# Optimization experiments

Hardware: AMD Instinct MI355X
Metric: run time of the kernel (lower is better)

The kernel has to match this reference:

```python
import jax, jax.numpy as jnp
import numpy as np
import math

EPS = 1e-5

def _ln(x, g, b):
    m = jnp.mean(x, axis=-1, keepdims=True)
    v = jnp.mean((x - m) ** 2, axis=-1, keepdims=True)
    return (x - m) * jax.lax.rsqrt(v + EPS) * g + b

def _heads(t, H):
    B, T, C = t.shape
    return t.reshape(B, T, H, C // H).transpose(0, 2, 1, 3)  # [B,H,T,D]

def _merge(t):
    B, H, T, D = t.shape
    return t.transpose(0, 2, 1, 3).reshape(B, T, H * D)

def _self_attn(x, w, b, pw, pb, H):
    B, T, C = x.shape
    q, k, v = jnp.split(x @ w + b, 3, axis=-1)
    q, k, v = _heads(q, H), _heads(k, H), _heads(v, H)
    D = C // H
    att = jnp.einsum('bhqd,bhkd->bhqk', q, k) * (1.0 / math.sqrt(D))
    causal = jnp.tril(jnp.ones((T, T), bool))
    att = jnp.where(causal[None, None], att, jnp.float32(-jnp.inf))
    att = jax.nn.softmax(att, axis=-1)
    out = _merge(jnp.einsum('bhqk,bhkd->bhqd', att, v))
    return out @ pw + pb

def _cross_attn(enc, dec, w, b, pw, pb, H):
    B, Td, C = dec.shape
    q_dec = jnp.split(dec @ w + b, 3, axis=-1)[0]
    _, k_enc, v_enc = jnp.split(enc @ w + b, 3, axis=-1)
    q = _heads(q_dec, H); k = _heads(k_enc, H); v = _heads(v_enc, H)
    D = C // H
    att = jnp.einsum('bhqd,bhkd->bhqk', q, k) * (1.0 / math.sqrt(D))
    att = jax.nn.softmax(att, axis=-1)
    out = _merge(jnp.einsum('bhqk,bhkd->bhqd', att, v))
    return out @ pw + pb

def _block(x, encoder_embd,
           ln1_g, ln1_b, ln2_g, ln2_b, ln3_g, ln3_b,
           attn_w, attn_b, aproj_w, aproj_b,
           ca_w, ca_b, caproj_w, caproj_b,
           fc_w, fc_b, mproj_w, mproj_b,
           down_w, down_b, up_w, up_b, H=16):
    x = x + _self_attn(_ln(x, ln1_g, ln1_b), attn_w, attn_b, aproj_w, aproj_b, H)
    x = x + _cross_attn(encoder_embd, _ln(x, ln2_g, ln2_b), ca_w, ca_b, caproj_w, caproj_b, H)
    h = jax.nn.gelu(_ln(x, ln3_g, ln3_b) @ fc_w + fc_b, approximate=True) @ mproj_w + mproj_b
    adapt = jax.nn.gelu(h @ down_w + down_b, approximate=True) @ up_w + up_b + h  # Adapter residual
    return x + adapt


def setup_inputs() -> dict:
    key = jax.random.key(0)
    ks = jax.random.split(key, 12)
    B, T, Te, C, H = 4, 1024, 257, 1024, 16
    s = 0.02
    f32 = jnp.float32
    return {
        'x': jax.random.normal(ks[0], (B, T, C), f32),
        'encoder_embd': jax.random.normal(ks[1], (B, Te, C), f32),
        'prefix_embd': jnp.zeros((B, 1, C), f32),
        'ln1_g': jnp.ones((C,), f32), 'ln1_b': jnp.zeros((C,), f32),
        'ln2_g': jnp.ones((C,), f32), 'ln2_b': jnp.zeros((C,), f32),
        'ln3_g': jnp.ones((C,), f32), 'ln3_b': jnp.zeros((C,), f32),
        'attn_w': jax.random.normal(ks[2], (C, 3 * C), f32) * s,
        'attn_b': jnp.zeros((3 * C,), f32),
        'aproj_w': jax.random.normal(ks[3], (C, C), f32) * s,
        'aproj_b': jnp.zeros((C,), f32),
        'ca_w': jax.random.normal(ks[4], (C, 3 * C), f32) * s,
        'ca_b': jnp.zeros((3 * C,), f32),
        'caproj_w': jax.random.normal(ks[5], (C, C), f32) * s,
        'caproj_b': jnp.zeros((C,), f32),
        'fc_w': jax.random.normal(ks[6], (C, 4 * C), f32) * s,
        'fc_b': jnp.zeros((4 * C,), f32),
        'mproj_w': jax.random.normal(ks[7], (4 * C, C), f32) * s,
        'mproj_b': jnp.zeros((C,), f32),
        'down_w': jax.random.normal(ks[8], (C, C // 4), f32) * s,
        'down_b': jnp.zeros((C // 4,), f32),
        'up_w': jax.random.normal(ks[9], (C // 4, C), f32) * s,
        'up_b': jnp.zeros((C,), f32),
    }


def reference(x, encoder_embd, prefix_embd,
              ln1_g, ln1_b, ln2_g, ln2_b, ln3_g, ln3_b,
              attn_w, attn_b, aproj_w, aproj_b,
              ca_w, ca_b, caproj_w, caproj_b,
              fc_w, fc_b, mproj_w, mproj_b,
              down_w, down_b, up_w, up_b):
    # prefix_embd unused (peft='adapter')
    return _block(x, encoder_embd,
                  ln1_g, ln1_b, ln2_g, ln2_b, ln3_g, ln3_b,
                  attn_w, attn_b, aproj_w, aproj_b,
                  ca_w, ca_b, caproj_w, caproj_b,
                  fc_w, fc_b, mproj_w, mproj_b,
                  down_w, down_b, up_w, up_b)
```

## Files before the change

kernel.cpp:

```cpp
#include <hip/hip_runtime.h>

typedef __attribute__((ext_vector_type(8))) short short8v;
typedef __attribute__((ext_vector_type(8))) unsigned short ushort8v;
typedef __attribute__((ext_vector_type(4))) unsigned short ushort4v;
typedef __attribute__((ext_vector_type(4))) float f32x4;

__device__ __forceinline__ unsigned short f2b(float f) {
  unsigned int u = __float_as_uint(f);
  unsigned int r = (u + 0x7FFFu + ((u >> 16) & 1u)) >> 16;
  return (unsigned short)r;
}
__device__ __forceinline__ float b2f(unsigned short h) {
  return __uint_as_float(((unsigned int)h) << 16);
}
__device__ __forceinline__ float gelu_f(float x) {
  float z = 0.7978845608028654f * (x + 0.044715f * x * x * x);
  float e = __expf(2.0f * z);
  float t = 1.0f - 2.0f / (e + 1.0f);
  return 0.5f * x * (1.0f + t);
}
__device__ __forceinline__ int xcd_swz(int wgid, int nwg) {
  int q = nwg >> 3, r = nwg & 7;
  int xcd = wgid & 7, idx = wgid >> 3;
  return (xcd < r ? xcd * (q + 1) : r * (q + 1) + (xcd - r) * q) + idx;
}

__global__ __launch_bounds__(256) void k_wprep(
    const float* aw, unsigned short* awt,
    const float* apw, unsigned short* apwt,
    const float* cw, unsigned short* cwt,
    const float* cpw, unsigned short* cpwt,
    const float* fw, unsigned short* fwt,
    const float* mw, unsigned short* mwt,
    const float* dw, unsigned short* dwt,
    const float* uw, unsigned short* uwt,
    const float* enc, unsigned short* encb) {
  __shared__ float tile[64][65];
  int bid = blockIdx.x, t = threadIdx.x;
  const float* w; unsigned short* wt; int K, N, gx, l;
  if      (bid < 768)  { w = aw;  wt = awt;  K = 1024; N = 3072; gx = 48; l = bid; }
  else if (bid < 1024) { w = apw; wt = apwt; K = 1024; N = 1024; gx = 16; l = bid - 768; }
  else if (bid < 1792) { w = cw;  wt = cwt;  K = 1024; N = 3072; gx = 48; l = bid - 1024; }
  else if (bid < 2048) { w = cpw; wt = cpwt; K = 1024; N = 1024; gx = 16; l = bid - 1792; }
  else if (bid < 3072) { w = fw;  wt = fwt;  K = 1024; N = 4096; gx = 64; l = bid - 2048; }
  else if (bid < 4096) { w = mw;  wt = mwt;  K = 4096; N = 1024; gx = 16; l = bid - 3072; }
  else if (bid < 4160) { w = dw;  wt = dwt;  K = 1024; N = 256;  gx = 4;  l = bid - 4096; }
  else if (bid < 4224) { w = uw;  wt = uwt;  K = 256;  N = 1024; gx = 16; l = bid - 4160; }
  else {
    size_t i = ((size_t)(bid - 4224) * 256 + t) * 4;
    f32x4 v = *(const f32x4*)&enc[i];
    ushort4v o;
#pragma unroll
    for (int j = 0; j < 4; ++j) o[j] = f2b(v[j]);
    *(ushort4v*)&encb[i] = o;
    return;
  }
  int bx = l % gx, by = l / gx;
  int tn = bx * 64, tk = by * 64;
  int c = t & 63, r0 = t >> 6;
#pragma unroll
  for (int p = 0; p < 16; ++p) {
    int r = r0 + p * 4;
    tile[r][c] = w[(size_t)(tk + r) * N + tn + c];
  }
  __syncthreads();
#pragma unroll
  for (int p = 0; p < 16; ++p) {
    int r = r0 + p * 4;
    wt[(size_t)(tn + r) * K + tk + c] = f2b(tile[c][r]);
  }
}

__global__ __launch_bounds__(256) void k_ln(const float* __restrict__ in,
                                            const float* __restrict__ g,
                                            const float* __restrict__ b,
                                            unsigned short* __restrict__ out) {
  int row = blockIdx.x;
  const float* x = in + (size_t)row * 1024;
  int t = threadIdx.x;
  float v0 = x[t], v1 = x[t + 256], v2 = x[t + 512], v3 = x[t + 768];
  float s = v0 + v1 + v2 + v3;
  float s2 = v0 * v0 + v1 * v1 + v2 * v2 + v3 * v3;
#pragma unroll
  for (int m = 1; m < 64; m <<= 1) { s += __shfl_xor(s, m); s2 += __shfl_xor(s2, m); }
  __shared__ float rs[4], rs2[4];
  int w = t >> 6;
  if ((t & 63) == 0) { rs[w] = s; rs2[w] = s2; }
  __syncthreads();
  s = rs[0] + rs[1] + rs[2] + rs[3];
  s2 = rs2[0] + rs2[1] + rs2[2] + rs2[3];
  float mean = s * (1.0f / 1024.0f);
  float var = s2 * (1.0f / 1024.0f) - mean * mean;
  float rinv = rsqrtf(var + 1e-5f);
  unsigned short* o = out + (size_t)row * 1024;
  o[t]       = f2b((v0 - mean) * rinv * g[t]       + b[t]);
  o[t + 256] = f2b((v1 - mean) * rinv * g[t + 256] + b[t + 256]);
  o[t + 512] = f2b((v2 - mean) * rinv * g[t + 512] + b[t + 512]);
  o[t + 768] = f2b((v3 - mean) * rinv * g[t + 768] + b[t + 768]);
}

template <bool GELU, bool WF32, bool WBF16, int NRES, bool RES1B>
__global__ __launch_bounds__(256, 2) void k_g128r(
    const unsigned short* __restrict__ A, int lda,
    const unsigned short* __restrict__ W, int ldw,
    const float* __restrict__ bias,
    const float* __restrict__ res1, const unsigned short* __restrict__ res1b,
    const float* __restrict__ res2,
    float* __restrict__ outF, unsigned short* __restrict__ outB,
    int M, int N, int K, int nbx) {
  __shared__ unsigned short lds[32768];
  const int t = threadIdx.x;
  const int swz = xcd_swz(blockIdx.x, gridDim.x);
  const int tileM = (swz / nbx) * 128, tileN = (swz % nbx) * 128;
  const int lane = t & 63, w = t >> 6;
  const int wm = (w >> 1) * 64, wn = (w & 1) * 64;
  const int lr16 = lane & 15, kc4 = lane >> 4;

  const int sr = t >> 1, hb = t & 1;
  int gr = tileM + sr; if (gr >= M) gr = M - 1;
  const unsigned short* ga = A + (size_t)gr * lda + hb * 32;
  const unsigned short* gw = W + (size_t)(tileN + sr) * ldw + hb * 32;
  unsigned short* const wbA = &lds[sr * 64];
  const int wsl[4] = {((hb * 4 + 0) ^ (sr & 7)) * 8, ((hb * 4 + 1) ^ (sr & 7)) * 8,
                      ((hb * 4 + 2) ^ (sr & 7)) * 8, ((hb * 4 + 3) ^ (sr & 7)) * 8};

  f32x4 acc[4][4];
#pragma unroll
  for (int i = 0; i < 4; ++i)
#pragma unroll
    for (int j = 0; j < 4; ++j) acc[i][j] = f32x4{0.f, 0.f, 0.f, 0.f};

  const int nt = K >> 6;
  ushort8v raE[4], rbE[4], raO[4], rbO[4];

#define LOADT(T, ra, rb)                                      \
  do {                                                        \
    int ko = (T) << 6;                                        \
    _Pragma("unroll") for (int j = 0; j < 4; ++j) {           \
      ra[j] = *(const ushort8v*)(ga + ko + j * 8);            \
      rb[j] = *(const ushort8v*)(gw + ko + j * 8);            \
    }                                                         \
  } while (0)
#define WRITET(ra, rb, bsel)                                  \
  do {                                                        \
    unsigned short* dA = wbA + (bsel) * 16384;                \
    _Pragma("unroll") for (int j = 0; j < 4; ++j) {           \
      *(ushort8v*)(dA + wsl[j]) = ra[j];                      \
      *(ushort8v*)(dA + 8192 + wsl[j]) = rb[j];               \
    }                                                         \
  } while (0)
#define COMPUTE(bsel)                                                           \
  do {                                                                          \
    const int base = (bsel) * 16384;                                            \
    _Pragma("unroll") for (int ks = 0; ks < 2; ++ks) {                          \
      short8v bfr[4];                                                           \
      _Pragma("unroll") for (int n = 0; n < 4; ++n) {                           \
        int r = wn + n * 16 + lr16;                                             \
        int sl = ((ks * 4 + kc4) ^ (r & 7)) * 8;                                \
        bfr[n] = *(const short8v*)&lds[base + 8192 + r * 64 + sl];              \
      }                                                                         \
      _Pragma("unroll") for (int mi = 0; mi < 4; ++mi) {                        \
        int r = wm + mi * 16 + lr16;                                            \
        int sl = ((ks * 4 + kc4) ^ (r & 7)) * 8;                                \
        short8v af = *(const short8v*)&lds[base + r * 64 + sl];                 \
        _Pragma("unroll") for (int n = 0; n < 4; ++n)                           \
          acc[mi][n] =                                                          \
              __builtin_amdgcn_mfma_f32_16x16x32_bf16(af, bfr[n], acc[mi][n], 0, 0, 0); \
      }                                                                         \
    }                                                                           \
  } while (0)

  LOADT(0, raE, rbE);
  WRITET(raE, rbE, 0);
  if (nt > 1) LOADT(1, raO, rbO);
  __syncthreads();

  for (int T = 0; T < nt; T += 2) {
    if (T + 2 < nt) LOADT(T + 2, raE, rbE);
    COMPUTE(0);
    if (T + 1 < nt) WRITET(raO, rbO, 1);
    __syncthreads();
    if (T + 1 < nt) {
      if (T + 3 < nt) LOADT(T + 3, raO, rbO);
      COMPUTE(1);
      if (T + 2 < nt) WRITET(raE, rbE, 0);
      __syncthreads();
    }
  }
#undef LOADT
#undef WRITET
#undef COMPUTE

#pragma unroll
  for (int mi = 0; mi < 4; ++mi) {
#pragma unroll
    for (int n = 0; n < 4; ++n) {
      int col = tileN + wn + n * 16 + lr16;
      float bv = bias[col];
#pragma unroll
      for (int qi = 0; qi < 4; ++qi) {
        int row = tileM + wm + mi * 16 + kc4 * 4 + qi;
        if (row < M) {
          float v = acc[mi][n][qi] + bv;
          if (GELU) v = gelu_f(v);
          size_t o = (size_t)row * N + col;
          if (NRES >= 1) v += RES1B ? b2f(res1b[o]) : res1[o];
          if (NRES >= 2) v += res2[o];
          if (WF32) outF[o] = v;
          if (WBF16) outB[o] = f2b(v);
        }
      }
    }
  }
}

__global__ __launch_bounds__(256) void k_vtrans(const unsigned short* __restrict__ src,
                                                int src_stride, int src_off, int TB,
                                                unsigned short* __restrict__ dst, int dst_tstride) {
  __shared__ unsigned short tile[64][72];
  int tb = blockIdx.x, bh = blockIdx.y;
  int b = bh >> 4, h = bh & 15;
  int t = threadIdx.x;
  int r = t >> 2, c0 = (t & 3) * 16;
  int tok = tb * 64 + r; if (tok >= TB) tok = TB - 1;
  const unsigned short* s = src + (size_t)(b * TB + tok) * src_stride + src_off + h * 64 + c0;
  *(ushort8v*)&tile[r][c0] = *(const ushort8v*)s;
  *(ushort8v*)&tile[r][c0 + 8] = *(const ushort8v*)(s + 8);
  __syncthreads();
  unsigned short tmp[16];
#pragma unroll
  for (int j = 0; j < 16; ++j) tmp[j] = tile[c0 + j][r];
  unsigned short* dp = dst + ((size_t)bh * 64 + r) * dst_tstride + tb * 64 + c0;
  *(ushort8v*)dp = *(const ushort8v*)&tmp[0];
  *(ushort8v*)(dp + 8) = *(const ushort8v*)&tmp[8];
}

template <bool CAUSAL>
__global__ __launch_bounds__(256) void k_attn(
    const unsigned short* __restrict__ Qb, int q_stride,
    const unsigned short* __restrict__ Kb, int k_stride, int k_off, int TKR,
    const unsigned short* __restrict__ Vt, int vt_tstride,
    unsigned short* __restrict__ out, int Tk) {
  __shared__ unsigned short Kl[64 * 72];
  __shared__ unsigned short Vl[64 * 72];
  __shared__ unsigned short Pl[4][16 * 72];
  const int swz = xcd_swz(blockIdx.x, gridDim.x);
  int qb = swz & 15, bh = swz >> 4;
  int b = bh >> 4, h = bh & 15;
  int t = threadIdx.x, lane = t & 63, w = t >> 6;
  int g = lane >> 4, lc = lane & 15;

  int qrow_g = qb * 64 + w * 16 + lc;
  const unsigned short* qp = Qb + (size_t)(b * 1024 + qrow_g) * q_stride + h * 64 + g * 8;
  short8v aq0 = *(const short8v*)qp;
  short8v aq1 = *(const short8v*)(qp + 32);

  f32x4 o[4];
  float m_[4], l_[4];
#pragma unroll
  for (int dt = 0; dt < 4; ++dt) o[dt] = f32x4{0.f, 0.f, 0.f, 0.f};
#pragma unroll
  for (int r = 0; r < 4; ++r) { m_[r] = -3.0e38f; l_[r] = 0.0f; }

  int srow = t >> 2;
  int sc = (t & 3) * 16;
  int ntiles = CAUSAL ? (qb + 1) : ((Tk + 63) >> 6);

  for (int kt = 0; kt < ntiles; ++kt) {
    __syncthreads();
    {
      int kg = kt * 64 + srow;
      if (!CAUSAL && kg >= Tk) kg = Tk - 1;
      const unsigned short* ks = Kb + (size_t)(b * TKR + kg) * k_stride + k_off + h * 64 + sc;
      *(ushort8v*)&Kl[srow * 72 + sc]     = *(const ushort8v*)ks;
      *(ushort8v*)&Kl[srow * 72 + sc + 8] = *(const ushort8v*)(ks + 8);
      const unsigned short* vs = Vt + ((size_t)bh * 64 + srow) * vt_tstride + kt * 64 + sc;
      *(ushort8v*)&Vl[srow * 72 + sc]     = *(const ushort8v*)vs;
      *(ushort8v*)&Vl[srow * 72 + sc + 8] = *(const ushort8v*)(vs + 8);
    }
    __syncthreads();

    f32x4 s[4];
#pragma unroll
    for (int jt = 0; jt < 4; ++jt) {
      short8v bk0 = *(const short8v*)&Kl[(jt * 16 + lc) * 72 + g * 8];
      short8v bk1 = *(const short8v*)&Kl[(jt * 16 + lc) * 72 + g * 8 + 32];
      f32x4 acc = f32x4{0.f, 0.f, 0.f, 0.f};
      acc = __builtin_amdgcn_mfma_f32_16x16x32_bf16(aq0, bk0, acc, 0, 0, 0);
      acc = __builtin_amdgcn_mfma_f32_16x16x32_bf16(aq1, bk1, acc, 0, 0, 0);
      s[jt] = acc;
    }
#pragma unroll
    for (int jt = 0; jt < 4; ++jt)
#pragma unroll
      for (int r = 0; r < 4; ++r) {
        float sv = s[jt][r] * 0.125f;
        bool masked = CAUSAL ? (kt == qb && (jt * 16 + lc) > (w * 16 + g * 4 + r))
                             : (kt * 64 + jt * 16 + lc >= Tk);
        s[jt][r] = masked ? -3.0e38f : sv;
      }
    float f[4];
#pragma unroll
    for (int r = 0; r < 4; ++r) {
      float mx = fmaxf(fmaxf(s[0][r], s[1][r]), fmaxf(s[2][r], s[3][r]));
      mx = fmaxf(mx, __shfl_xor(mx, 1));
      mx = fmaxf(mx, __shfl_xor(mx, 2));
      mx = fmaxf(mx, __shfl_xor(mx, 4));
      mx = fmaxf(mx, __shfl_xor(mx, 8));
      float mnew = fmaxf(m_[r], mx);
      f[r] = __expf(m_[r] - mnew);
      m_[r] = mnew;
      float rsum = 0.0f;
#pragma unroll
      for (int jt = 0; jt < 4; ++jt) {
        float p = __expf(s[jt][r] - mnew);
        s[jt][r] = p;
        rsum += p;
      }
      rsum += __shfl_xor(rsum, 1);
      rsum += __shfl_xor(rsum, 2);
      rsum += __shfl_xor(rsum, 4);
      rsum += __shfl_xor(rsum, 8);
      l_[r] = l_[r] * f[r] + rsum;
    }
#pragma unroll
    for (int dt = 0; dt < 4; ++dt)
#pragma unroll
      for (int r = 0; r < 4; ++r) o[dt][r] *= f[r];
#pragma unroll
    for (int jt = 0; jt < 4; ++jt)
#pragma unroll
      for (int r = 0; r < 4; ++r)
        Pl[w][(g * 4 + r) * 72 + jt * 16 + lc] = f2b(s[jt][r]);
    short8v ap0 = *(const short8v*)&Pl[w][lc * 72 + g * 8];
    short8v ap1 = *(const short8v*)&Pl[w][lc * 72 + g * 8 + 32];
#pragma unroll
    for (int dt = 0; dt < 4; ++dt) {
      short8v bv0 = *(const short8v*)&Vl[(dt * 16 + lc) * 72 + g * 8];
      short8v bv1 = *(const short8v*)&Vl[(dt * 16 + lc) * 72 + g * 8 + 32];
      o[dt] = __builtin_amdgcn_mfma_f32_16x16x32_bf16(ap0, bv0, o[dt], 0, 0, 0);
      o[dt] = __builtin_amdgcn_mfma_f32_16x16x32_bf16(ap1, bv1, o[dt], 0, 0, 0);
    }
  }
  size_t orow = (size_t)(b * 1024 + qb * 64 + w * 16) * 1024 + h * 64;
#pragma unroll
  for (int r = 0; r < 4; ++r) {
    float inv = 1.0f / l_[r];
#pragma unroll
    for (int dt = 0; dt < 4; ++dt)
      out[orow + (size_t)(g * 4 + r) * 1024 + dt * 16 + lc] = f2b(o[dt][r] * inv);
  }
}

extern "C" void kernel_launch(void* const* d_in, const int* in_sizes, int n_in,
                              void* d_out, int out_size, void* d_ws, size_t ws_size,
                              hipStream_t stream) {
  (void)in_sizes; (void)n_in; (void)out_size; (void)ws_size;
  const float* x       = (const float*)d_in[0];
  const float* enc     = (const float*)d_in[1];
  const float* ln1_g   = (const float*)d_in[3];
  const float* ln1_b   = (const float*)d_in[4];
  const float* ln2_g   = (const float*)d_in[5];
  const float* ln2_b   = (const float*)d_in[6];
  const float* ln3_g   = (const float*)d_in[7];
  const float* ln3_b   = (const float*)d_in[8];
  const float* attn_w  = (const float*)d_in[9];
  const float* attn_b  = (const float*)d_in[10];
  const float* aproj_w = (const float*)d_in[11];
  const float* aproj_b = (const float*)d_in[12];
  const float* ca_w    = (const float*)d_in[13];
  const float* ca_b    = (const float*)d_in[14];
  const float* caproj_w= (const float*)d_in[15];
  const float* caproj_b= (const float*)d_in[16];
  const float* fc_w    = (const float*)d_in[17];
  const float* fc_b    = (const float*)d_in[18];
  const float* mproj_w = (const float*)d_in[19];
  const float* mproj_b = (const float*)d_in[20];
  const float* down_w  = (const float*)d_in[21];
  const float* down_b  = (const float*)d_in[22];
  const float* up_w    = (const float*)d_in[23];
  const float* up_b    = (const float*)d_in[24];
  float* out = (float*)d_out;
  char* ws = (char*)d_ws;

  const size_t O_WATTN = 0, O_WAPROJ = 6291456, O_WCA = 8388608, O_WCAPROJ = 14680064,
               O_WFC = 16777216, O_WMPROJ = 25165824, O_WDOWN = 33554432, O_WUP = 34078720,
               O_ENC = 34603008, O_LN = 36708352, O_BIG = 45096960,
               O_XRES = 78651392, O_ATTN = 112205824;

  unsigned short* wt_attn   = (unsigned short*)(ws + O_WATTN);
  unsigned short* wt_aproj  = (unsigned short*)(ws + O_WAPROJ);
  unsigned short* wt_ca     = (unsigned short*)(ws + O_WCA);
  unsigned short* wt_caproj = (unsigned short*)(ws + O_WCAPROJ);
  unsigned short* wt_fc     = (unsigned short*)(ws + O_WFC);
  unsigned short* wt_mproj  = (unsigned short*)(ws + O_WMPROJ);
  unsigned short* wt_down   = (unsigned short*)(ws + O_WDOWN);
  unsigned short* wt_up     = (unsigned short*)(ws + O_WUP);
  unsigned short* encbf     = (unsigned short*)(ws + O_ENC);
  unsigned short* lnout     = (unsigned short*)(ws + O_LN);
  unsigned short* hbf       = (unsigned short*)(ws + O_LN);
  unsigned short* qkvb      = (unsigned short*)(ws + O_BIG);
  unsigned short* vt_self   = (unsigned short*)(ws + O_BIG + 25165824);
  unsigned short* q2b       = (unsigned short*)(ws + O_BIG);
  unsigned short* kvb       = (unsigned short*)(ws + O_BIG + 8388608);
  unsigned short* vt_cross  = (unsigned short*)(ws + O_BIG + 12599296);
  unsigned short* caout     = (unsigned short*)(ws + O_BIG + 15220736);
  unsigned short* fcout     = (unsigned short*)(ws + O_BIG);
  float*          xres      = (float*)(ws + O_XRES);
  unsigned short* attnout   = (unsigned short*)(ws + O_ATTN);
  unsigned short* dmid      = (unsigned short*)(ws + O_ATTN);

  dim3 blk(256);

  k_wprep<<<dim3(5252), blk, 0, stream>>>(
      attn_w, wt_attn, aproj_w, wt_aproj, ca_w, wt_ca, caproj_w, wt_caproj,
      fc_w, wt_fc, mproj_w, wt_mproj, down_w, wt_down, up_w, wt_up, enc, encbf);

  k_ln<<<dim3(4096), blk, 0, stream>>>(x, ln1_g, ln1_b, lnout);
  k_g128r<false, false, true, 0, false><<<dim3(768), blk, 0, stream>>>(
      lnout, 1024, wt_attn, 1024, attn_b, nullptr, nullptr, nullptr, nullptr, qkvb,
      4096, 3072, 1024, 24);
  k_vtrans<<<dim3(16, 64), blk, 0, stream>>>(qkvb, 3072, 2048, 1024, vt_self, 1024);
  k_attn<true><<<dim3(1024), blk, 0, stream>>>(
      qkvb, 3072, qkvb, 3072, 1024, 1024, vt_self, 1024, attnout, 1024);
  k_g128r<false, true, false, 1, false><<<dim3(256), blk, 0, stream>>>(
      attnout, 1024, wt_aproj, 1024, aproj_b, x, nullptr, nullptr, xres, nullptr,
      4096, 1024, 1024, 8);

  k_ln<<<dim3(4096), blk, 0, stream>>>(xres, ln2_g, ln2_b, lnout);
  k_g128r<false, false, true, 0, false><<<dim3(256), blk, 0, stream>>>(
      lnout, 1024, wt_ca, 1024, ca_b, nullptr, nullptr, nullptr, nullptr, q2b,
      4096, 1024, 1024, 8);
  k_g128r<false, false, true, 0, false><<<dim3(144), blk, 0, stream>>>(
      encbf, 1024, wt_ca + (size_t)1024 * 1024, 1024, ca_b + 1024, nullptr, nullptr,
      nullptr, nullptr, kvb, 1028, 2048, 1024, 16);
  k_vtrans<<<dim3(5, 64), blk, 0, stream>>>(kvb, 2048, 1024, 257, vt_cross, 320);
  k_attn<false><<<dim3(1024), blk, 0, stream>>>(
      q2b, 1024, kvb, 2048, 0, 257, vt_cross, 320, caout, 257);
  k_g128r<false, true, false, 1, false><<<dim3(256), blk, 0, stream>>>(
      caout, 1024, wt_caproj, 1024, caproj_b, xres, nullptr, nullptr, xres, nullptr,
      4096, 1024, 1024, 8);

  k_ln<<<dim3(4096), blk, 0, stream>>>(xres, ln3_g, ln3_b, lnout);
  k_g128r<true, false, true, 0, false><<<dim3(1024), blk, 0, stream>>>(
      lnout, 1024, wt_fc, 1024, fc_b, nullptr, nullptr, nullptr, nullptr, fcout,
      4096, 4096, 1024, 32);
  k_g128r<false, false, true, 0, false><<<dim3(256), blk, 0, stream>>>(
      fcout, 4096, wt_mproj, 4096, mproj_b, nullptr, nullptr, nullptr, nullptr, hbf,
      4096, 1024, 4096, 8);

  k_g128r<true, false, true, 0, false><<<dim3(64), blk, 0, stream>>>(
      hbf, 1024, wt_down, 1024, down_b, nullptr, nullptr, nullptr, nullptr, dmid,
      4096, 256, 1024, 2);
  k_g128r<false, true, false, 2, true><<<dim3(256), blk, 0, stream>>>(
      dmid, 256, wt_up, 256, up_b, nullptr, hbf, xres, out, nullptr,
      4096, 1024, 256, 8);
}
```

Before: 456.2 us.

## Single-buffer GEMM LDS for higher occupancy and remap tiles per XCD

The 128x128 GEMM kernel moves from a double-buffered LDS tile (64KB) to a single buffer (32KB) and raises launch_bounds occupancy from 2 to 4 blocks per CU. The aim is to hide memory latency with more resident waves instead of intra-block double buffering. The cost is extra __syncthreads per K step, since writes and computes on the one buffer must now be serialised. A new tile mapping gives each XCD a contiguous 2D region of output tiles for better L2 reuse, falling back to the old swizzle when the grid shape does not divide evenly.

```diff
diff --git a/kernel.cpp b/kernel.cpp
--- a/kernel.cpp
+++ b/kernel.cpp
@@ -23,6 +23,20 @@
   int q = nwg >> 3, r = nwg & 7;
   int xcd = wgid & 7, idx = wgid >> 3;
   return (xcd < r ? xcd * (q + 1) : r * (q + 1) + (xcd - r) * q) + idx;
+}
+__device__ __forceinline__ void map_tile(int wgid, int nwg, int nbx, int& tm, int& tn) {
+  int nby = nwg / nbx;
+  if ((nwg & 7) == 0 && (nby & 3) == 0 && (nbx & 1) == 0) {
+    int x = wgid & 7, idx = wgid >> 3;
+    int rh = nby >> 2, rw = nbx >> 1;
+    int xr = x >> 1, xc = x & 1;
+    tm = xr * rh + idx / rw;
+    tn = xc * rw + idx % rw;
+  } else {
+    int swz = xcd_swz(wgid, nwg);
+    tm = swz / nbx;
+    tn = swz % nbx;
+  }
 }
 
 __global__ __launch_bounds__(256) void k_wprep(
@@ -100,7 +114,7 @@
 }
 
 template <bool GELU, bool WF32, bool WBF16, int NRES, bool RES1B>
-__global__ __launch_bounds__(256, 2) void k_g128r(
+__global__ __launch_bounds__(256, 4) void k_g128r(
     const unsigned short* __restrict__ A, int lda,
     const unsigned short* __restrict__ W, int ldw,
     const float* __restrict__ bias,
@@ -108,10 +122,11 @@
     const float* __restrict__ res2,
     float* __restrict__ outF, unsigned short* __restrict__ outB,
     int M, int N, int K, int nbx) {
-  __shared__ unsigned short lds[32768];
+  __shared__ unsigned short lds[16384];
   const int t = threadIdx.x;
-  const int swz = xcd_swz(blockIdx.x, gridDim.x);
-  const int tileM = (swz / nbx) * 128, tileN = (swz % nbx) * 128;
+  int tm, tn;
+  map_tile(blockIdx.x, gridDim.x, nbx, tm, tn);
+  const int tileM = tm * 128, tileN = tn * 128;
   const int lane = t & 63, w = t >> 6;
   const int wm = (w >> 1) * 64, wn = (w & 1) * 64;
   const int lr16 = lane & 15, kc4 = lane >> 4;
@@ -141,28 +156,26 @@
       rb[j] = *(const ushort8v*)(gw + ko + j * 8);            \
     }                                                         \
   } while (0)
-#define WRITET(ra, rb, bsel)                                  \
+#define WRITET(ra, rb)                                        \
   do {                                                        \
-    unsigned short* dA = wbA + (bsel) * 16384;                \
     _Pragma("unroll") for (int j = 0; j < 4; ++j) {           \
-      *(ushort8v*)(dA + wsl[j]) = ra[j];                      \
-      *(ushort8v*)(dA + 8192 + wsl[j]) = rb[j];               \
+      *(ushort8v*)(wbA + wsl[j]) = ra[j];                     \
+      *(ushort8v*)(wbA + 8192 + wsl[j]) = rb[j];              \
     }                                                         \
   } while (0)
-#define COMPUTE(bsel)                                                           \
+#define COMPUTE()                                                               \
   do {                                                                          \
-    const int base = (bsel) * 16384;                                            \
     _Pragma("unroll") for (int ks = 0; ks < 2; ++ks) {                          \
       short8v bfr[4];                                                           \
       _Pragma("unroll") for (int n = 0; n < 4; ++n) {                           \
         int r = wn + n * 16 + lr16;                                             \
         int sl = ((ks * 4 + kc4) ^ (r & 7)) * 8;                                \
-        bfr[n] = *(const short8v*)&lds[base + 8192 + r * 64 + sl];              \
+        bfr[n] = *(const short8v*)&lds[8192 + r * 64 + sl];                     \
       }                                                                         \
       _Pragma("unroll") for (int mi = 0; mi < 4; ++mi) {                        \
         int r = wm + mi * 16 + lr16;                                            \
         int sl = ((ks * 4 + kc4) ^ (r & 7)) * 8;                                \
-        short8v af = *(const short8v*)&lds[base + r * 64 + sl];                 \
+        short8v af = *(const short8v*)&lds[r * 64 + sl];                        \
         _Pragma("unroll") for (int n = 0; n < 4; ++n)                           \
           acc[mi][n] =                                                          \
               __builtin_amdgcn_mfma_f32_16x16x32_bf16(af, bfr[n], acc[mi][n], 0, 0, 0); \
@@ -171,19 +184,21 @@
   } while (0)
 
   LOADT(0, raE, rbE);
-  WRITET(raE, rbE, 0);
+  WRITET(raE, rbE);
   if (nt > 1) LOADT(1, raO, rbO);
   __syncthreads();
 
   for (int T = 0; T < nt; T += 2) {
     if (T + 2 < nt) LOADT(T + 2, raE, rbE);
-    COMPUTE(0);
-    if (T + 1 < nt) WRITET(raO, rbO, 1);
+    COMPUTE();
     __syncthreads();
     if (T + 1 < nt) {
+      WRITET(raO, rbO);
       if (T + 3 < nt) LOADT(T + 3, raO, rbO);
-      COMPUTE(1);
-      if (T + 2 < nt) WRITET(raE, rbE, 0);
+      __syncthreads();
+      COMPUTE();
+      __syncthreads();
+      if (T + 2 < nt) WRITET(raE, rbE);
       __syncthreads();
     }
   }
```

Result: slower. 793.9 us (+74.0%).

## Split-K the mproj and adapter-down GEMMs with a reduction kernel, add 2D XCD tile mapping

Applied to the files above, without the earlier changes.

The mproj GEMM (K=4096, 256 tiles) and the adapter down-projection (64 tiles) each split K four ways, write fp32 partials to a new workspace region, and a new reduction kernel sums them, adds bias, applies GELU where needed and writes bf16. This raises workgroup count so these small-tile-count GEMMs can fill the GPU, at the cost of extra fp32 partial traffic and an additional launch. A new tile mapper also assigns each XCD a contiguous 2D block of output tiles when the grid shape allows, aiming for better L2 reuse of A and W. The split path only runs if the workspace is large enough, otherwise the old path is used.

```diff
diff --git a/kernel.cpp b/kernel.cpp
--- a/kernel.cpp
+++ b/kernel.cpp
@@ -23,6 +23,20 @@
   int q = nwg >> 3, r = nwg & 7;
   int xcd = wgid & 7, idx = wgid >> 3;
   return (xcd < r ? xcd * (q + 1) : r * (q + 1) + (xcd - r) * q) + idx;
+}
+__device__ __forceinline__ void map_tile(int wgid, int nwg, int nbx, int& tm, int& tn) {
+  int nby = nwg / nbx;
+  if ((nwg & 7) == 0 && (nby & 3) == 0 && (nbx & 1) == 0) {
+    int x = wgid & 7, idx = wgid >> 3;
+    int rh = nby >> 2, rw = nbx >> 1;
+    int xr = x >> 1, xc = x & 1;
+    tm = xr * rh + idx / rw;
+    tn = xc * rw + idx % rw;
+  } else {
+    int swz = xcd_swz(wgid, nwg);
+    tm = swz / nbx;
+    tn = swz % nbx;
+  }
 }
 
 __global__ __launch_bounds__(256) void k_wprep(
@@ -99,7 +113,7 @@
   o[t + 768] = f2b((v3 - mean) * rinv * g[t + 768] + b[t + 768]);
 }
 
-template <bool GELU, bool WF32, bool WBF16, int NRES, bool RES1B>
+template <bool GELU, bool BIAS, bool WF32, bool WBF16, int NRES, bool RES1B>
 __global__ __launch_bounds__(256, 2) void k_g128r(
     const unsigned short* __restrict__ A, int lda,
     const unsigned short* __restrict__ W, int ldw,
@@ -107,19 +121,24 @@
     const float* __restrict__ res1, const unsigned short* __restrict__ res1b,
     const float* __restrict__ res2,
     float* __restrict__ outF, unsigned short* __restrict__ outB,
-    int M, int N, int K, int nbx) {
+    int M, int N, int K, int nbx, int splitk, size_t zO) {
   __shared__ unsigned short lds[32768];
   const int t = threadIdx.x;
-  const int swz = xcd_swz(blockIdx.x, gridDim.x);
-  const int tileM = (swz / nbx) * 128, tileN = (swz % nbx) * 128;
+  const int nsub = gridDim.x / splitk;
+  const int split = blockIdx.x / nsub;
+  const int sub = blockIdx.x % nsub;
+  int tm, tn;
+  map_tile(sub, nsub, nbx, tm, tn);
+  const int tileM = tm * 128, tileN = tn * 128;
+  const int Keff = K / splitk;
   const int lane = t & 63, w = t >> 6;
   const int wm = (w >> 1) * 64, wn = (w & 1) * 64;
   const int lr16 = lane & 15, kc4 = lane >> 4;
 
   const int sr = t >> 1, hb = t & 1;
   int gr = tileM + sr; if (gr >= M) gr = M - 1;
-  const unsigned short* ga = A + (size_t)gr * lda + hb * 32;
-  const unsigned short* gw = W + (size_t)(tileN + sr) * ldw + hb * 32;
+  const unsigned short* ga = A + (size_t)gr * lda + (size_t)split * Keff + hb * 32;
+  const unsigned short* gw = W + (size_t)(tileN + sr) * ldw + (size_t)split * Keff + hb * 32;
   unsigned short* const wbA = &lds[sr * 64];
   const int wsl[4] = {((hb * 4 + 0) ^ (sr & 7)) * 8, ((hb * 4 + 1) ^ (sr & 7)) * 8,
                       ((hb * 4 + 2) ^ (sr & 7)) * 8, ((hb * 4 + 3) ^ (sr & 7)) * 8};
@@ -130,7 +149,7 @@
 #pragma unroll
     for (int j = 0; j < 4; ++j) acc[i][j] = f32x4{0.f, 0.f, 0.f, 0.f};
 
-  const int nt = K >> 6;
+  const int nt = Keff >> 6;
   ushort8v raE[4], rbE[4], raO[4], rbO[4];
 
 #define LOADT(T, ra, rb)                                      \
@@ -191,12 +210,13 @@
 #undef WRITET
 #undef COMPUTE
 
+  if (WF32 && splitk > 1) outF += (size_t)split * zO;
 #pragma unroll
   for (int mi = 0; mi < 4; ++mi) {
 #pragma unroll
     for (int n = 0; n < 4; ++n) {
       int col = tileN + wn + n * 16 + lr16;
-      float bv = bias[col];
+      float bv = BIAS ? bias[col] : 0.0f;
 #pragma unroll
       for (int qi = 0; qi < 4; ++qi) {
         int row = tileM + wm + mi * 16 + kc4 * 4 + qi;
@@ -212,6 +232,22 @@
       }
     }
   }
+}
+
+template <bool GELU, int NM1>
+__global__ __launch_bounds__(256) void k_red(const float* __restrict__ p,
+                                             const float* __restrict__ bias,
+                                             unsigned short* __restrict__ ob, size_t S) {
+  size_t i = ((size_t)blockIdx.x * 256 + threadIdx.x) * 4;
+  f32x4 v = *(const f32x4*)&p[i];
+  v += *(const f32x4*)&p[i + S];
+  v += *(const f32x4*)&p[i + 2 * S];
+  v += *(const f32x4*)&p[i + 3 * S];
+  v += *(const f32x4*)&bias[i & NM1];
+  ushort4v o;
+#pragma unroll
+  for (int j = 0; j < 4; ++j) o[j] = f2b(GELU ? gelu_f(v[j]) : v[j]);
+  *(ushort4v*)&ob[i] = o;
 }
 
 __global__ __launch_bounds__(256) void k_vtrans(const unsigned short* __restrict__ src,
@@ -355,7 +391,7 @@
 extern "C" void kernel_launch(void* const* d_in, const int* in_sizes, int n_in,
                               void* d_out, int out_size, void* d_ws, size_t ws_size,
                               hipStream_t stream) {
-  (void)in_sizes; (void)n_in; (void)out_size; (void)ws_size;
+  (void)in_sizes; (void)n_in; (void)out_size;
   const float* x       = (const float*)d_in[0];
   const float* enc     = (const float*)d_in[1];
   const float* ln1_g   = (const float*)d_in[3];
@@ -386,7 +422,7 @@
   const size_t O_WATTN = 0, O_WAPROJ = 6291456, O_WCA = 8388608, O_WCAPROJ = 14680064,
                O_WFC = 16777216, O_WMPROJ = 25165824, O_WDOWN = 33554432, O_WUP = 34078720,
                O_ENC = 34603008, O_LN = 36708352, O_BIG = 45096960,
-               O_XRES = 78651392, O_ATTN = 112205824;
+               O_XRES = 78651392, O_ATTN = 112205824, O_PART = 121634816;
 
   unsigned short* wt_attn   = (unsigned short*)(ws + O_WATTN);
   unsigned short* wt_aproj  = (unsigned short*)(ws + O_WAPROJ);
@@ -409,6 +445,9 @@
   float*          xres      = (float*)(ws + O_XRES);
   unsigned short* attnout   = (unsigned short*)(ws + O_ATTN);
   unsigned short* dmid      = (unsigned short*)(ws + O_ATTN);
+  float*          part      = (float*)(ws + O_PART);
+
+  bool splitok = ws_size >= O_PART + 67108864;
 
   dim3 blk(256);
 
@@ -417,42 +456,58 @@
       fc_w, wt_fc, mproj_w, wt_mproj, down_w, wt_down, up_w, wt_up, enc, encbf);
 
   k_ln<<<dim3(4096), blk, 0, stream>>>(x, ln1_g, ln1_b, lnout);
-  k_g128r<false, false, true, 0, false><<<dim3(768), blk, 0, stream>>>(
+  k_g128r<false, true, false, true, 0, false><<<dim3(768), blk, 0, stream>>>(
       lnout, 1024, wt_attn, 1024, attn_b, nullptr, nullptr, nullptr, nullptr, qkvb,
-      4096, 3072, 1024, 24);
+      4096, 3072, 1024, 24, 1, 0);
   k_vtrans<<<dim3(16, 64), blk, 0, stream>>>(qkvb, 3072, 2048, 1024, vt_self, 1024);
   k_attn<true><<<dim3(1024), blk, 0, stream>>>(
       qkvb, 3072, qkvb, 3072, 1024, 1024, vt_self, 1024, attnout, 1024);
-  k_g128r<false, true, false, 1, false><<<dim3(256), blk, 0, stream>>>(
+  k_g128r<false, true, true, false, 1, false><<<dim3(256), blk, 0, stream>>>(
       attnout, 1024, wt_aproj, 1024, aproj_b, x, nullptr, nullptr, xres, nullptr,
-      4096, 1024, 1024, 8);
+      4096, 1024, 1024, 8, 1, 0);
 
   k_ln<<<dim3(4096), blk, 0, stream>>>(xres, ln2_g, ln2_b, lnout);
-  k_g128r<false, false, true, 0, false><<<dim3(256), blk, 0, stream>>>(
+  k_g128r<false, true, false, true, 0, false><<<dim3(256), blk, 0, stream>>>(
       lnout, 1024, wt_ca, 1024, ca_b, nullptr, nullptr, nullptr, nullptr, q2b,
-      4096, 1024, 1024, 8);
-  k_g128r<false, false, true, 0, false><<<dim3(144), blk, 0, stream>>>(
+      4096, 1024, 1024, 8, 1, 0);
+  k_g128r<false, true, false, true, 0, false><<<dim3(144), blk, 0, stream>>>(
       encbf, 1024, wt_ca + (size_t)1024 * 1024, 1024, ca_b + 1024, nullptr, nullptr,
-      nullptr, nullptr, kvb, 1028, 2048, 1024, 16);
+      nullptr, nullptr, kvb, 1028, 2048, 1024, 16, 1, 0);
   k_vtrans<<<dim3(5, 64), blk, 0, stream>>>(kvb, 2048, 1024, 257, vt_cross, 320);
   k_attn<false><<<dim3(1024), blk, 0, stream>>>(
       q2b, 1024, kvb, 2048, 0, 257, vt_cross, 320, caout, 257);
-  k_g128r<false, true, false, 1, false><<<dim3(256), blk, 0, stream>>>(
+  k_g128r<false, true, true, false, 1, false><<<dim3(256), blk, 0, stream>>>(
       caout, 1024, wt_caproj, 1024, caproj_b, xres, nullptr, nullptr, xres, nullptr,
-      4096, 1024, 1024, 8);
+      4096, 1024, 1024, 8, 1, 0);
 
   k_ln<<<dim3(4096), blk, 0, stream>>>(xres, ln3_g, ln3_b, lnout);
-  k_g128r<true, false, true, 0, false><<<dim3(1024), blk, 0, stream>>>(
+  k_g128r<true, true, false, true, 0, false><<<dim3(1024), blk, 0, stream>>>(
       lnout, 1024, wt_fc, 1024, fc_b, nullptr, nullptr, nullptr, nullptr, fcout,
-      4096, 4096, 1024, 32);
-  k_g128r<false, false, true, 0, false><<<dim3(256), blk, 0, stream>>>(
-      fcout, 4096, wt_mproj, 4096, mproj_b, nullptr, nullptr, nullptr, nullptr, hbf,
-      4096, 1024, 4096, 8);
-
-  k_g128r<true, false, true, 0, false><<<dim3(64), blk, 0, stream>>>(
-      hbf, 1024, wt_down, 1024, down_b, nullptr, nullptr, nullptr, nullptr, dmid,
-      4096, 256, 1024, 2);
-  k_g128r<false, true, false, 2, true><<<dim3(256), blk, 0, stream>>>(
+      4096, 4096, 1024, 32, 1, 0);
+  if (splitok) {
+    k_g128r<false, false, true, false, 0, false><<<dim3(1024), blk, 0, stream>>>(
+        fcout, 4096, wt_mproj, 4096, nullptr, nullptr, nullptr, nullptr, part, nullptr,
+        4096, 1024, 4096, 8, 4, (size_t)4096 * 1024);
+    k_red<false, 1023><<<dim3(4096), blk, 0, stream>>>(part, mproj_b, hbf,
+                                                       (size_t)4096 * 1024);
+  } else {
+    k_g128r<false, true, false, true, 0, false><<<dim3(256), blk, 0, stream>>>(
+        fcout, 4096, wt_mproj, 4096, mproj_b, nullptr, nullptr, nullptr, nullptr, hbf,
+        4096, 1024, 4096, 8, 1, 0);
+  }
+
+  if (splitok) {
+    k_g128r<false, false, true, false, 0, false><<<dim3(256), blk, 0, stream>>>(
+        hbf, 1024, wt_down, 1024, nullptr, nullptr, nullptr, nullptr, part, nullptr,
+        4096, 256, 1024, 2, 4, (size_t)4096 * 256);
+    k_red<true, 255><<<dim3(1024), blk, 0, stream>>>(part, down_b, dmid,
+                                                     (size_t)4096 * 256);
+  } else {
+    k_g128r<true, true, false, true, 0, false><<<dim3(64), blk, 0, stream>>>(
+        hbf, 1024, wt_down, 1024, down_b, nullptr, nullptr, nullptr, nullptr, dmid,
+        4096, 256, 1024, 2, 1, 0);
+  }
+  k_g128r<false, true, true, false, 2, true><<<dim3(256), blk, 0, stream>>>(
       dmid, 256, wt_up, 256, up_b, nullptr, hbf, xres, out, nullptr,
-      4096, 1024, 256, 8);
-}
+      4096, 1024, 256, 8, 1, 0);
+}
```

Result: slower. 471.9 us (+3.5%).
